# Kernel optimization log

Hardware: AMD Instinct MI355X
Metric: run time of the kernel (lower is better)

Reference implementation:

```python
import jax, jax.numpy as jnp
import numpy as np

HARDLIM_THRESH = 0.2


def setup_inputs() -> dict:
    key = jax.random.key(0)
    k_inp, k_w1, k_b1, k_w2, k_b2 = jax.random.split(key, 5)
    B, D, H, F = 16384, 4096, 2048, 512
    scale1 = 1.0 / np.sqrt(D)
    scale2 = 1.0 / np.sqrt(H)
    return {
        "inp": jax.random.normal(k_inp, (B, D), dtype=jnp.float32),
        "W1": jax.random.normal(k_w1, (H, D), dtype=jnp.float32) * scale1,
        "b1": jax.random.normal(k_b1, (H,), dtype=jnp.float32) * scale1,
        "W2": jax.random.normal(k_w2, (F, H), dtype=jnp.float32) * scale2,
        "b2": jax.random.normal(k_b2, (F,), dtype=jnp.float32) * scale2,
        "k": 8,
    }


def reference(inp, W1, b1, W2, b2, k):
    # Linear -> ReLU -> Linear
    h = jax.nn.relu(inp @ W1.T + b1)            # [B, H]
    logits = h @ W2.T + b2                      # [B, F]
    # 'hard' attention: sigmoid -> keep top-k (zero the rest) -> hardlim(0.2)
    s = jax.nn.sigmoid(logits)
    topk_vals, _ = jax.lax.top_k(s, k)          # [B, k]
    kth = topk_vals[:, -1:]                     # per-row k-th largest value
    gated = jnp.where(s >= kth, s, 0.0)         # GetTopK: zero non-top-k entries
    out = jnp.where(gated > HARDLIM_THRESH, 1.0, 0.0).astype(inp.dtype)
    return out
```

## Files before the change

kernel.cpp:

```cpp
#include <hip/hip_runtime.h>
#include <math.h>
#include <type_traits>


#define BM 128
#define BN 128
#define BK 16

#define TAU   1.0e-4f
#define L02F -1.3862943611198906f

typedef __attribute__((ext_vector_type(8))) short  bf16x8;
typedef __attribute__((ext_vector_type(8))) ushort u16x8;
typedef __attribute__((ext_vector_type(4))) float  f32x4;

__device__ inline ushort bfhi(float f)   { return (ushort)(__float_as_uint(f) >> 16); }
__device__ inline float  bfhif(float f)  { return __uint_as_float(__float_as_uint(f) & 0xFFFF0000u); }

__device__ inline void gload_lds16(const void* g, void* l) {
    __builtin_amdgcn_global_load_lds(
        (const __attribute__((address_space(1))) unsigned int*)g,
        (__attribute__((address_space(3))) unsigned int*)l, 16, 0, 0);
}

__global__ __launch_bounds__(256) void split_kernel(
    const float* __restrict__ src, ushort* __restrict__ hi,
    ushort* __restrict__ lo, size_t n4, int* cnt)
{
    if (cnt && blockIdx.x == 0 && threadIdx.x == 0) *cnt = 0;
    size_t i = (size_t)blockIdx.x * 256 + threadIdx.x;
    size_t stride = (size_t)gridDim.x * 256;
    for (; i < n4; i += stride) {
        float4 v = ((const float4*)src)[i];
        ushort4 h, l;
        h.x = bfhi(v.x); l.x = bfhi(v.x - bfhif(v.x));
        h.y = bfhi(v.y); l.y = bfhi(v.y - bfhif(v.y));
        h.z = bfhi(v.z); l.z = bfhi(v.z - bfhif(v.z));
        h.w = bfhi(v.w); l.w = bfhi(v.w - bfhif(v.w));
        ((ushort4*)hi)[i] = h;
        ((ushort4*)lo)[i] = l;
    }
}

__global__ __launch_bounds__(512, 2) void bgemm1_256(
    const ushort* __restrict__ aH, const ushort* __restrict__ aL,
    const ushort* __restrict__ wH, const ushort* __restrict__ wL,
    const float* __restrict__ b1,
    ushort* __restrict__ Chi, ushort* __restrict__ Clo)
{
    __shared__ ushort lds[65536];
    const int t    = threadIdx.x;
    const int lane = t & 63;
    const int wave = t >> 6;
    const int wr   = wave >> 1;
    const int wc   = wave & 1;
    const int l15  = lane & 15;
    const int l4   = lane >> 4;

    const int bid = blockIdx.x;
    const int xcd = bid & 7;
    const int j   = bid >> 3;
    const int bm  = xcd * 8 + (j >> 3);
    const int bn  = j & 7;

    const int cq = lane & 3;
    const int r0 = wave * 32 + (lane >> 2);
    const int r1 = r0 + 16;
    const size_t sw0 = (size_t)((cq ^ ((r0 >> 1) & 3)) * 8);
    const size_t sw1 = (size_t)((cq ^ ((r1 >> 1) & 3)) * 8);
    const size_t gA0 = (size_t)(bm * 256 + r0) * 4096 + sw0;
    const size_t gA1 = (size_t)(bm * 256 + r1) * 4096 + sw1;
    const size_t gB0 = (size_t)(bn * 256 + r0) * 4096 + sw0;
    const size_t gB1 = (size_t)(bn * 256 + r1) * 4096 + sw1;

    f32x4 acc[4][8];
    #pragma unroll
    for (int mi = 0; mi < 4; ++mi)
        #pragma unroll
        for (int ni = 0; ni < 8; ++ni)
            acc[mi][ni] = (f32x4){0.f, 0.f, 0.f, 0.f};

    auto stage = [&](int b, int kt) {
        const size_t ko = (size_t)kt * 32;
        ushort* L0 = &lds[b * 32768];
        gload_lds16(aH + gA0 + ko, L0 + wave * 1024);
        gload_lds16(aH + gA1 + ko, L0 + wave * 1024 + 512);
        gload_lds16(aL + gA0 + ko, L0 + 8192 + wave * 1024);
        gload_lds16(aL + gA1 + ko, L0 + 8192 + wave * 1024 + 512);
        gload_lds16(wH + gB0 + ko, L0 + 16384 + wave * 1024);
        gload_lds16(wH + gB1 + ko, L0 + 16384 + wave * 1024 + 512);
        gload_lds16(wL + gB0 + ko, L0 + 24576 + wave * 1024);
        gload_lds16(wL + gB1 + ko, L0 + 24576 + wave * 1024 + 512);
    };
    auto compute = [&](int b) {
        const ushort* L0 = &lds[b * 32768];
        bf16x8 ah[4], al[4];
        #pragma unroll
        for (int mi = 0; mi < 4; ++mi) {
            int row = wr * 64 + mi * 16 + l15;
            int o = row * 32 + ((l4 ^ ((row >> 1) & 3)) << 3);
            ah[mi] = *(const bf16x8*)&L0[o];
            al[mi] = *(const bf16x8*)&L0[8192 + o];
        }
        #pragma unroll
        for (int h = 0; h < 2; ++h) {
            bf16x8 bh[4], bl[4];
            #pragma unroll
            for (int q = 0; q < 4; ++q) {
                int row = wc * 128 + (h * 4 + q) * 16 + l15;
                int o = row * 32 + ((l4 ^ ((row >> 1) & 3)) << 3);
                bh[q] = *(const bf16x8*)&L0[16384 + o];
                bl[q] = *(const bf16x8*)&L0[24576 + o];
            }
            __builtin_amdgcn_s_setprio(1);
            #pragma unroll
            for (int mi = 0; mi < 4; ++mi)
                #pragma unroll
                for (int q = 0; q < 4; ++q) {
                    acc[mi][h * 4 + q] = __builtin_amdgcn_mfma_f32_16x16x32_bf16(ah[mi], bh[q], acc[mi][h * 4 + q], 0, 0, 0);
                    acc[mi][h * 4 + q] = __builtin_amdgcn_mfma_f32_16x16x32_bf16(ah[mi], bl[q], acc[mi][h * 4 + q], 0, 0, 0);
                    acc[mi][h * 4 + q] = __builtin_amdgcn_mfma_f32_16x16x32_bf16(al[mi], bh[q], acc[mi][h * 4 + q], 0, 0, 0);
                }
            __builtin_amdgcn_s_setprio(0);
        }
    };

    stage(0, 0);
    asm volatile("s_waitcnt vmcnt(0)");
    __builtin_amdgcn_s_barrier();

    const int nt = 128;
    for (int kt = 0; kt < nt - 1; ++kt) {
        stage((kt + 1) & 1, kt + 1);
        __builtin_amdgcn_sched_barrier(0);
        compute(kt & 1);
        asm volatile("s_waitcnt vmcnt(0)");
        asm volatile("s_waitcnt lgkmcnt(0)\n\ts_barrier" ::: "memory");
    }
    compute((nt - 1) & 1);

    #pragma unroll
    for (int ni = 0; ni < 8; ++ni) {
        int col = bn * 256 + wc * 128 + ni * 16 + l15;
        float bv = b1[col];
        #pragma unroll
        for (int mi = 0; mi < 4; ++mi) {
            int rowb = bm * 256 + wr * 64 + mi * 16 + l4 * 4;
            #pragma unroll
            for (int r = 0; r < 4; ++r) {
                float v = fmaxf(acc[mi][ni][r] + bv, 0.0f);
                size_t idx = (size_t)(rowb + r) * 2048 + col;
                Chi[idx] = bfhi(v);
                Clo[idx] = bfhi(v - bfhif(v));
            }
        }
    }
}

template<int OUT_SPLIT>
__global__ __launch_bounds__(512, 2) void bgemm_glds(
    const ushort* __restrict__ aH, const ushort* __restrict__ aL,
    const ushort* __restrict__ wH, const ushort* __restrict__ wL,
    const float* __restrict__ bias,
    ushort* __restrict__ Chi, ushort* __restrict__ Clo,
    float* __restrict__ C32,
    int N, int K, int nbm, int nbn)
{
    __shared__ ushort lds[73728];
    const int t    = threadIdx.x;
    const int lane = t & 63;
    const int wave = t >> 6;
    const int wr   = wave >> 1;
    const int wc   = wave & 1;
    const int l15  = lane & 15;
    const int l4   = lane >> 4;

    const int bid = blockIdx.x;
    const int xcd = bid & 7;
    const int j   = bid >> 3;
    const int bm  = xcd * (nbm >> 3) + j / nbn;
    const int bn  = j % nbn;

    const int c   = lane & 3;
    const int rA0 = (wave * 2 + 0) * 16 + (lane >> 2);
    const int rA1 = (wave * 2 + 1) * 16 + (lane >> 2);
    const int rB  = wave * 16 + (lane >> 2);
    const size_t offA0 = (size_t)(bm * 256 + rA0) * K + (size_t)((c ^ ((rA0 >> 1) & 3)) * 8);
    const size_t offA1 = (size_t)(bm * 256 + rA1) * K + (size_t)((c ^ ((rA1 >> 1) & 3)) * 8);
    const size_t offB  = (size_t)(bn * 128 + rB ) * K + (size_t)((c ^ ((rB  >> 1) & 3)) * 8);
    const ushort* sAh0 = aH + offA0; const ushort* sAl0 = aL + offA0;
    const ushort* sAh1 = aH + offA1; const ushort* sAl1 = aL + offA1;
    const ushort* sBh  = wH + offB;  const ushort* sBl  = wL + offB;

    f32x4 acc[4][4];
    #pragma unroll
    for (int mi = 0; mi < 4; ++mi)
        #pragma unroll
        for (int ni = 0; ni < 4; ++ni)
            acc[mi][ni] = (f32x4){0.f, 0.f, 0.f, 0.f};

    auto stage = [&](int b, int kt) {
        const size_t ko = (size_t)kt * 32;
        ushort* L0 = &lds[b * 24576];
        gload_lds16(sAh0 + ko, L0 + (wave * 2 + 0) * 512);
        gload_lds16(sAh1 + ko, L0 + (wave * 2 + 1) * 512);
        gload_lds16(sAl0 + ko, L0 + 8192 + (wave * 2 + 0) * 512);
        gload_lds16(sAl1 + ko, L0 + 8192 + (wave * 2 + 1) * 512);
        gload_lds16(sBh + ko,  L0 + 16384 + wave * 512);
        gload_lds16(sBl + ko,  L0 + 20480 + wave * 512);
    };
    auto frag_read = [&](int b, bf16x8 ah[4], bf16x8 al[4], bf16x8 bh[4], bf16x8 bl[4]) {
        const ushort* L0 = &lds[b * 24576];
        #pragma unroll
        for (int mi = 0; mi < 4; ++mi) {
            int row = wr * 64 + mi * 16 + l15;
            int o = row * 32 + ((l4 ^ ((row >> 1) & 3)) << 3);
            ah[mi] = *(const bf16x8*)&L0[o];
            al[mi] = *(const bf16x8*)&L0[8192 + o];
        }
        #pragma unroll
        for (int ni = 0; ni < 4; ++ni) {
            int row = wc * 64 + ni * 16 + l15;
            int o = row * 32 + ((l4 ^ ((row >> 1) & 3)) << 3);
            bh[ni] = *(const bf16x8*)&L0[16384 + o];
            bl[ni] = *(const bf16x8*)&L0[20480 + o];
        }
    };
    auto do_mfma = [&](bf16x8 ah[4], bf16x8 al[4], bf16x8 bh[4], bf16x8 bl[4]) {
        __builtin_amdgcn_s_setprio(1);
        #pragma unroll
        for (int mi = 0; mi < 4; ++mi)
            #pragma unroll
            for (int ni = 0; ni < 4; ++ni) {
                acc[mi][ni] = __builtin_amdgcn_mfma_f32_16x16x32_bf16(ah[mi], bh[ni], acc[mi][ni], 0, 0, 0);
                acc[mi][ni] = __builtin_amdgcn_mfma_f32_16x16x32_bf16(ah[mi], bl[ni], acc[mi][ni], 0, 0, 0);
                acc[mi][ni] = __builtin_amdgcn_mfma_f32_16x16x32_bf16(al[mi], bh[ni], acc[mi][ni], 0, 0, 0);
            }
        __builtin_amdgcn_s_setprio(0);
    };

    stage(0, 0);
    stage(1, 1);
    asm volatile("s_waitcnt vmcnt(6)");
    __builtin_amdgcn_s_barrier();

    const int nt = K / 32;
    bf16x8 ah[4], al[4], bh[4], bl[4];

    for (int kt = 0; kt < nt - 2; ++kt) {
        frag_read(kt % 3, ah, al, bh, bl);
        stage((kt + 2) % 3, kt + 2);
        __builtin_amdgcn_sched_barrier(0);
        do_mfma(ah, al, bh, bl);
        asm volatile("s_waitcnt vmcnt(6)");
        asm volatile("s_waitcnt lgkmcnt(0)\n\ts_barrier" ::: "memory");
    }
    {
        frag_read((nt - 2) % 3, ah, al, bh, bl);
        do_mfma(ah, al, bh, bl);
        asm volatile("s_waitcnt vmcnt(0)");
        asm volatile("s_waitcnt lgkmcnt(0)\n\ts_barrier" ::: "memory");
    }
    {
        frag_read((nt - 1) % 3, ah, al, bh, bl);
        do_mfma(ah, al, bh, bl);
    }

    #pragma unroll
    for (int ni = 0; ni < 4; ++ni) {
        int col = bn * 128 + wc * 64 + ni * 16 + l15;
        float bv = bias[col];
        #pragma unroll
        for (int mi = 0; mi < 4; ++mi) {
            int rowb = bm * 256 + wr * 64 + mi * 16 + l4 * 4;
            #pragma unroll
            for (int r = 0; r < 4; ++r) {
                float v = acc[mi][ni][r] + bv;
                size_t idx = (size_t)(rowb + r) * N + col;
                if (OUT_SPLIT) {
                    v = fmaxf(v, 0.0f);
                    Chi[idx] = bfhi(v);
                    Clo[idx] = bfhi(v - bfhif(v));
                } else {
                    C32[idx] = v;
                }
            }
        }
    }
}

__global__ __launch_bounds__(256) void repair_r1(
    const float* __restrict__ inp,
    const float* __restrict__ W1, const float* __restrict__ b1,
    double* __restrict__ h64,
    const int* __restrict__ risky, const int* __restrict__ cnt, int maxr)
{
    int c = *cnt; if (c > maxr) c = maxr;
    const int by = blockIdx.y;
    if (by * 8 >= c) return;
    __shared__ float Xs[8][4096];
    const int t = threadIdx.x;

    int ridx[8];
    #pragma unroll
    for (int r = 0; r < 8; ++r) {
        int slot = by * 8 + r;
        ridx[r] = risky[slot < c ? slot : (c - 1)];
    }
    #pragma unroll
    for (int i = 0; i < 32; ++i) {
        int lin = t + i * 256;
        int r = lin >> 10, q = lin & 1023;
        *(float4*)&Xs[r][q * 4] = *(const float4*)(inp + (size_t)ridx[r] * 4096 + q * 4);
    }
    __syncthreads();

    const int n0 = blockIdx.x * 256 + t;
    const float* w0 = W1 + (size_t)n0 * 4096;
    double acc[8] = {};

    for (int k = 0; k < 4096; k += 4) {
        float4 a0 = *(const float4*)(w0 + k);
        float xr[8][4];
        #pragma unroll
        for (int r = 0; r < 8; ++r)
            *(float4*)&xr[r][0] = *(const float4*)&Xs[r][k];
        const float* ap0 = &a0.x;
        #pragma unroll
        for (int j = 0; j < 4; ++j) {
            double wd0 = (double)ap0[j];
            #pragma unroll
            for (int r = 0; r < 8; ++r)
                acc[r] = fma(wd0, (double)xr[r][j], acc[r]);
        }
    }

    double bv0 = (double)b1[n0];
    #pragma unroll
    for (int r = 0; r < 8; ++r) {
        int slot = by * 8 + r;
        if (slot < c)
            h64[(size_t)slot * 2048 + n0] = fmax(acc[r] + bv0, 0.0);
    }
}

__global__ __launch_bounds__(256) void repair_r2(
    const double* __restrict__ h64,
    const float* __restrict__ W2, const float* __restrict__ b2,
    double* __restrict__ L64,
    const int* __restrict__ cnt, int maxr)
{
    int c = *cnt; if (c > maxr) c = maxr;
    const int by = blockIdx.y;
    if (by * 4 >= c) return;
    __shared__ double Xs[4][2048];
    const int t = threadIdx.x;

    #pragma unroll
    for (int i = 0; i < 16; ++i) {
        int lin = t + i * 256;
        int r = lin >> 10, q = lin & 1023;
        int slot = by * 4 + r; if (slot >= c) slot = c - 1;
        *(double2*)&Xs[r][q * 2] = *(const double2*)(h64 + (size_t)slot * 2048 + q * 2);
    }
    __syncthreads();

    const int n0 = t;
    const int n1 = t + 256;
    const float* w0 = W2 + (size_t)n0 * 2048;
    const float* w1 = W2 + (size_t)n1 * 2048;
    double acc[2][4] = {};

    for (int k = 0; k < 2048; k += 4) {
        float4 a0 = *(const float4*)(w0 + k);
        float4 a1 = *(const float4*)(w1 + k);
        double xr[4][4];
        #pragma unroll
        for (int r = 0; r < 4; ++r) {
            *(double2*)&xr[r][0] = *(const double2*)&Xs[r][k];
            *(double2*)&xr[r][2] = *(const double2*)&Xs[r][k + 2];
        }
        const float* ap0 = &a0.x;
        const float* ap1 = &a1.x;
        #pragma unroll
        for (int j = 0; j < 4; ++j) {
            double wd0 = (double)ap0[j];
            double wd1 = (double)ap1[j];
            #pragma unroll
            for (int r = 0; r < 4; ++r) {
                acc[0][r] = fma(wd0, xr[r][j], acc[0][r]);
                acc[1][r] = fma(wd1, xr[r][j], acc[1][r]);
            }
        }
    }

    double bv0 = (double)b2[n0], bv1 = (double)b2[n1];
    #pragma unroll
    for (int r = 0; r < 4; ++r) {
        int slot = by * 4 + r;
        if (slot < c) {
            L64[(size_t)slot * 512 + n0] = acc[0][r] + bv0;
            L64[(size_t)slot * 512 + n1] = acc[1][r] + bv1;
        }
    }
}

template<typename TA, int MODE>
__global__ __launch_bounds__(256, 1) void gemm64(
    const TA* __restrict__ A, int lda,
    const float* __restrict__ W, int ldw,
    const float* __restrict__ bias,
    double* __restrict__ out64, int N, int K)
{
    __shared__ double As[BK][BM + 2];
    __shared__ double Bs[BK][BN + 2];
    const int t  = threadIdx.x;
    const int tm = t >> 4;
    const int tn = t & 15;
    const size_t bm = blockIdx.x;
    const size_t bn = blockIdx.y;
    const TA*    Ab = A + bm * BM * (size_t)lda;
    const float* Wb = W + bn * BN * (size_t)ldw;

    double acc[8][8] = {};

    for (int k0 = 0; k0 < K; k0 += BK) {
        #pragma unroll
        for (int i = 0; i < 2; ++i) {
            int f   = t + i * 256;
            int row = f >> 2;
            int kc  = (f & 3) << 2;
            if constexpr (std::is_same<TA, double>::value) {
                double2 v0 = *(const double2*)(Ab + (size_t)row * lda + k0 + kc);
                double2 v1 = *(const double2*)(Ab + (size_t)row * lda + k0 + kc + 2);
                As[kc + 0][row] = v0.x; As[kc + 1][row] = v0.y;
                As[kc + 2][row] = v1.x; As[kc + 3][row] = v1.y;
            } else {
                float4 va = *(const float4*)(Ab + (size_t)row * lda + k0 + kc);
                As[kc + 0][row] = (double)va.x; As[kc + 1][row] = (double)va.y;
                As[kc + 2][row] = (double)va.z; As[kc + 3][row] = (double)va.w;
            }
            float4 vb = *(const float4*)(Wb + (size_t)row * ldw + k0 + kc);
            Bs[kc + 0][row] = (double)vb.x; Bs[kc + 1][row] = (double)vb.y;
            Bs[kc + 2][row] = (double)vb.z; Bs[kc + 3][row] = (double)vb.w;
        }
        __syncthreads();
        #pragma unroll
        for (int k = 0; k < BK; ++k) {
            double a[8], b[8];
            #pragma unroll
            for (int i = 0; i < 4; ++i) {
                *(double2*)&a[i * 2] = *(const double2*)&As[k][tm * 8 + i * 2];
                *(double2*)&b[i * 2] = *(const double2*)&Bs[k][tn * 8 + i * 2];
            }
            #pragma unroll
            for (int i = 0; i < 8; ++i)
                #pragma unroll
                for (int j = 0; j < 8; ++j)
                    acc[i][j] = fma(a[i], b[j], acc[i][j]);
        }
        __syncthreads();
    }

    double bv[8];
    if (MODE != 2) {
        #pragma unroll
        for (int j = 0; j < 8; ++j) bv[j] = (double)bias[bn * BN + tn * 8 + j];
    }

    #pragma unroll
    for (int i = 0; i < 8; ++i) {
        size_t row  = bm * BM + (size_t)tm * 8 + i;
        size_t base = row * (size_t)N + bn * BN + tn * 8;
        #pragma unroll
        for (int j = 0; j < 8; ++j) {
            double v = acc[i][j];
            if (MODE == 0) out64[base + j] = fmax(v + bv[j], 0.0);
            if (MODE == 1) out64[base + j] = v + bv[j];
            if (MODE == 2) out64[base + j] += v;
        }
    }
}

__global__ __launch_bounds__(256) void margin_topk32(
    const float* L, float* O, int ncols,
    const int* __restrict__ kp, int* __restrict__ risky, int* __restrict__ cnt,
    int maxr)
{
    const int wave = threadIdx.x >> 6;
    const int lane = threadIdx.x & 63;
    const int k = *kp;
    const size_t row = (size_t)blockIdx.x * 4 + wave;
    const float* Lr = L + row * (size_t)ncols;

    float v[8];
    *(float4*)&v[0] = *(const float4*)(Lr + lane * 8);
    *(float4*)&v[4] = *(const float4*)(Lr + lane * 8 + 4);
    float w[8];
    #pragma unroll
    for (int j = 0; j < 8; ++j) w[j] = v[j];

    float kth = -3.0e38f, minD = 3.0e38f;
    for (int it = 0; it < k; ++it) {
        float mv = w[0]; int mj = 0;
        #pragma unroll
        for (int j = 1; j < 8; ++j)
            if (w[j] > mv) { mv = w[j]; mj = j; }
        int mi = lane * 8 + mj;
        #pragma unroll
        for (int off = 32; off; off >>= 1) {
            float ov = __shfl_xor(mv, off);
            int   oi = __shfl_xor(mi, off);
            if (ov > mv || (ov == mv && oi < mi)) { mv = ov; mi = oi; }
        }
        kth = mv;
        minD = fminf(minD, fabsf(mv - L02F));
        if ((mi >> 3) == lane) w[mi & 7] = -3.0e38f;
    }
    float nv = w[0];
    #pragma unroll
    for (int j = 1; j < 8; ++j) nv = fmaxf(nv, w[j]);
    #pragma unroll
    for (int off = 32; off; off >>= 1) nv = fmaxf(nv, __shfl_xor(nv, off));

    bool risk = ((kth - nv) < 2.0f * TAU) || (minD < TAU);
    if (risk && lane == 0) {
        int p = atomicAdd(cnt, 1);
        if (p < maxr) risky[p] = (int)row;
    }

    float o[8];
    #pragma unroll
    for (int j = 0; j < 8; ++j)
        o[j] = (v[j] >= kth && v[j] > L02F) ? 1.0f : 0.0f;
    float* Op = O + row * (size_t)ncols + lane * 8;
    *(float4*)&Op[0] = *(const float4*)&o[0];
    *(float4*)&Op[4] = *(const float4*)&o[4];
}

__global__ __launch_bounds__(256) void topk64_kernel(
    const double* __restrict__ L, float* __restrict__ O, int ncols,
    const int* __restrict__ kp,
    const int* __restrict__ risky, const int* __restrict__ cnt, int maxr)
{
    const int wave = threadIdx.x >> 6;
    const int lane = threadIdx.x & 63;
    const int k = *kp;
    size_t pos = (size_t)blockIdx.x * 4 + wave;
    size_t row = pos;
    if (cnt) {
        int c = *cnt; if (c > maxr) c = maxr;
        if ((int)pos >= c) return;
        row = (size_t)risky[pos];
    }
    const double* Lr = L + pos * (size_t)ncols;

    double v[8];
    #pragma unroll
    for (int j = 0; j < 8; ++j) {
        double l = Lr[lane * 8 + j];
        v[j] = 1.0 / (1.0 + exp(-l));
    }
    double w[8];
    #pragma unroll
    for (int j = 0; j < 8; ++j) w[j] = v[j];

    double kth = -1.0e300;
    for (int it = 0; it < k; ++it) {
        double mv = w[0]; int mj = 0;
        #pragma unroll
        for (int j = 1; j < 8; ++j)
            if (w[j] > mv) { mv = w[j]; mj = j; }
        int mi = lane * 8 + mj;
        #pragma unroll
        for (int off = 32; off; off >>= 1) {
            double ov = __shfl_xor(mv, off);
            int    oi = __shfl_xor(mi, off);
            if (ov > mv || (ov == mv && oi < mi)) { mv = ov; mi = oi; }
        }
        kth = mv;
        if ((mi >> 3) == lane) w[mi & 7] = -1.0e300;
    }

    float o[8];
    #pragma unroll
    for (int j = 0; j < 8; ++j)
        o[j] = (v[j] >= kth && v[j] > 0.2) ? 1.0f : 0.0f;
    float* Op = O + row * (size_t)ncols + lane * 8;
    *(float4*)&Op[0] = *(const float4*)&o[0];
    *(float4*)&Op[4] = *(const float4*)&o[4];
}

extern "C" void kernel_launch(void* const* d_in, const int* in_sizes, int n_in,
                              void* d_out, int out_size, void* d_ws, size_t ws_size,
                              hipStream_t stream) {
    const float* inp = (const float*)d_in[0];
    const float* W1  = (const float*)d_in[1];
    const float* b1  = (const float*)d_in[2];
    const float* W2  = (const float*)d_in[3];
    const float* b2  = (const float*)d_in[4];
    const int*   kp  = (const int*)d_in[5];

    const int H = in_sizes[2];
    const int F = in_sizes[4];
    const int D = in_sizes[1] / H;
    const int B = in_sizes[0] / D;
    float* out = (float*)d_out;

    const int MAXR = 8192;
    const size_t szHpair = (size_t)B * H * 4;
    const size_t szW1p   = (size_t)H * D * 4;
    const size_t szW2p   = (size_t)F * H * 4;
    const size_t szInpP  = (size_t)B * D * 4;
    const size_t needMain = szHpair + szW1p + szW2p + (size_t)MAXR * 4 + 256;
    const size_t needA    = needMain + szInpP;
    const bool shapeOK = (D == 4096 && H == 2048 && F == 512 && B == 16384);

    if (shapeOK && ws_size >= needA) {
        ushort* h_hi  = (ushort*)d_ws;
        ushort* h_lo  = h_hi + (size_t)B * H;
        ushort* w1h   = (ushort*)((char*)d_ws + szHpair);
        ushort* w1l   = w1h + (size_t)H * D;
        ushort* w2h   = (ushort*)((char*)d_ws + szHpair + szW1p);
        ushort* w2l   = w2h + (size_t)F * H;
        int*    risky = (int*)((char*)d_ws + szHpair + szW1p + szW2p);
        int*    cnt   = risky + MAXR;
        ushort* inH   = (ushort*)((char*)d_ws + needMain);
        ushort* inL   = inH + (size_t)B * D;
        double* h64   = (double*)d_ws;
        double* L64   = (double*)((char*)d_ws + szHpair);
        float*  l32   = out;

        split_kernel<<<2048, 256, 0, stream>>>(W1, w1h, w1l, (size_t)H * D / 4, cnt);
        split_kernel<<<512, 256, 0, stream>>>(W2, w2h, w2l, (size_t)F * H / 4, nullptr);
        split_kernel<<<4096, 256, 0, stream>>>(inp, inH, inL, (size_t)B * D / 4, nullptr);
        bgemm1_256<<<512, 512, 0, stream>>>(inH, inL, w1h, w1l, b1, h_hi, h_lo);
        bgemm_glds<0><<<256, 512, 0, stream>>>(
            h_hi, h_lo, w2h, w2l, b2, nullptr, nullptr, l32, F, H, B / 256, F / 128);
        margin_topk32<<<B / 4, 256, 0, stream>>>(l32, out, F, kp, risky, cnt, MAXR);
        repair_r1<<<dim3(8, MAXR / 8), 256, 0, stream>>>(
            inp, W1, b1, h64, risky, cnt, MAXR);
        repair_r2<<<dim3(1, MAXR / 4), 256, 0, stream>>>(
            h64, W2, b2, L64, cnt, MAXR);
        topk64_kernel<<<MAXR / 4, 256, 0, stream>>>(L64, out, F, kp, risky, cnt, MAXR);
    } else {
        int Hc = H, Bc = 0;
        for (;;) {
            size_t perRow = (size_t)F * 8 + (size_t)Hc * 8;
            Bc = (int)((ws_size / perRow) / BM) * BM;
            if (Bc >= BM || Hc <= BM) break;
            Hc >>= 1;
        }
        if (Bc < BM) Bc = BM;
        if (Bc > B)  Bc = B;
        double* L   = (double*)d_ws;
        double* h64 = L + (size_t)Bc * F;

        for (int b0 = 0; b0 < B; b0 += Bc) {
            int bc = (B - b0 < Bc) ? (B - b0) : Bc;
            for (int h0 = 0; h0 < H; h0 += Hc) {
                int hc = (H - h0 < Hc) ? (H - h0) : Hc;
                gemm64<float, 0><<<dim3(bc / BM, hc / BN), 256, 0, stream>>>(
                    inp + (size_t)b0 * D, D, W1 + (size_t)h0 * D, D, b1 + h0,
                    h64, hc, D);
                if (h0 == 0)
                    gemm64<double, 1><<<dim3(bc / BM, F / BN), 256, 0, stream>>>(
                        h64, hc, W2 + h0, H, b2, L, F, hc);
                else
                    gemm64<double, 2><<<dim3(bc / BM, F / BN), 256, 0, stream>>>(
                        h64, hc, W2 + h0, H, b2, L, F, hc);
            }
            topk64_kernel<<<bc / 4, 256, 0, stream>>>(
                L, out + (size_t)b0 * F, F, kp, nullptr, nullptr, 0);
        }
    }
}
```

Before: 1.237 ms.

## Load GEMM1 A operand directly into registers, stage only B through LDS

The first GEMM now fetches its A-tile fragments (hi and lo bf16 splits) straight from global memory into VGPRs with inline global_load_dwordx4, instead of staging them through LDS. Only the W1 tile is double-buffered in LDS, which halves shared memory per block and removes the LDS write/read traffic for A. The cost is that each pair of waves sharing a row band loads the same A data redundantly from global/L2. The A loads are also issued in the same iteration they are consumed, with only a partial vmcnt wait, so their latency is exposed rather than prefetched.

```diff
diff --git a/kernel.cpp b/kernel.cpp
--- a/kernel.cpp
+++ b/kernel.cpp
@@ -42,13 +42,13 @@
     }
 }
 
-__global__ __launch_bounds__(512, 2) void bgemm1_256(
+__global__ __launch_bounds__(512, 2) void bgemm1_areg(
     const ushort* __restrict__ aH, const ushort* __restrict__ aL,
     const ushort* __restrict__ wH, const ushort* __restrict__ wL,
     const float* __restrict__ b1,
     ushort* __restrict__ Chi, ushort* __restrict__ Clo)
 {
-    __shared__ ushort lds[65536];
+    __shared__ ushort lds[32768];
     const int t    = threadIdx.x;
     const int lane = t & 63;
     const int wave = t >> 6;
@@ -64,14 +64,13 @@
     const int bn  = j & 7;
 
     const int cq = lane & 3;
-    const int r0 = wave * 32 + (lane >> 2);
-    const int r1 = r0 + 16;
-    const size_t sw0 = (size_t)((cq ^ ((r0 >> 1) & 3)) * 8);
-    const size_t sw1 = (size_t)((cq ^ ((r1 >> 1) & 3)) * 8);
-    const size_t gA0 = (size_t)(bm * 256 + r0) * 4096 + sw0;
-    const size_t gA1 = (size_t)(bm * 256 + r1) * 4096 + sw1;
-    const size_t gB0 = (size_t)(bn * 256 + r0) * 4096 + sw0;
-    const size_t gB1 = (size_t)(bn * 256 + r1) * 4096 + sw1;
+    const int rs0 = wave * 32 + (lane >> 2);
+    const int rs1 = rs0 + 16;
+    const size_t gB0 = (size_t)(bn * 256 + rs0) * 4096 + (size_t)((cq ^ ((rs0 >> 1) & 3)) * 8);
+    const size_t gB1 = (size_t)(bn * 256 + rs1) * 4096 + (size_t)((cq ^ ((rs1 >> 1) & 3)) * 8);
+
+    const ushort* aHb = aH + ((size_t)(bm * 256 + wr * 64 + l15)) * 4096 + l4 * 8;
+    const ushort* aLb = aL + ((size_t)(bm * 256 + wr * 64 + l15)) * 4096 + l4 * 8;
 
     f32x4 acc[4][8];
     #pragma unroll
@@ -80,64 +79,76 @@
         for (int ni = 0; ni < 8; ++ni)
             acc[mi][ni] = (f32x4){0.f, 0.f, 0.f, 0.f};
 
-    auto stage = [&](int b, int kt) {
+    auto stageB = [&](int b, int kt) {
         const size_t ko = (size_t)kt * 32;
-        ushort* L0 = &lds[b * 32768];
-        gload_lds16(aH + gA0 + ko, L0 + wave * 1024);
-        gload_lds16(aH + gA1 + ko, L0 + wave * 1024 + 512);
-        gload_lds16(aL + gA0 + ko, L0 + 8192 + wave * 1024);
-        gload_lds16(aL + gA1 + ko, L0 + 8192 + wave * 1024 + 512);
-        gload_lds16(wH + gB0 + ko, L0 + 16384 + wave * 1024);
-        gload_lds16(wH + gB1 + ko, L0 + 16384 + wave * 1024 + 512);
-        gload_lds16(wL + gB0 + ko, L0 + 24576 + wave * 1024);
-        gload_lds16(wL + gB1 + ko, L0 + 24576 + wave * 1024 + 512);
+        ushort* L0 = &lds[b * 16384];
+        gload_lds16(wH + gB0 + ko, L0 + wave * 1024);
+        gload_lds16(wH + gB1 + ko, L0 + wave * 1024 + 512);
+        gload_lds16(wL + gB0 + ko, L0 + 8192 + wave * 1024);
+        gload_lds16(wL + gB1 + ko, L0 + 8192 + wave * 1024 + 512);
     };
-    auto compute = [&](int b) {
-        const ushort* L0 = &lds[b * 32768];
-        bf16x8 ah[4], al[4];
+    auto a_load = [&](int kt, bf16x8 av[8]) {
+        const size_t ko = (size_t)kt * 32;
         #pragma unroll
         for (int mi = 0; mi < 4; ++mi) {
-            int row = wr * 64 + mi * 16 + l15;
+            asm volatile("global_load_dwordx4 %0, %1, off"
+                         : "=v"(av[mi])     : "v"(aHb + ko + (size_t)mi * 65536));
+            asm volatile("global_load_dwordx4 %0, %1, off"
+                         : "=v"(av[4 + mi]) : "v"(aLb + ko + (size_t)mi * 65536));
+        }
+    };
+    auto mfma_half = [&](int b, int h, bf16x8 av[8]) {
+        const ushort* L0 = &lds[b * 16384];
+        bf16x8 bh[4], bl[4];
+        #pragma unroll
+        for (int q = 0; q < 4; ++q) {
+            int row = wc * 128 + (h * 4 + q) * 16 + l15;
             int o = row * 32 + ((l4 ^ ((row >> 1) & 3)) << 3);
-            ah[mi] = *(const bf16x8*)&L0[o];
-            al[mi] = *(const bf16x8*)&L0[8192 + o];
-        }
-        #pragma unroll
-        for (int h = 0; h < 2; ++h) {
-            bf16x8 bh[4], bl[4];
+            bh[q] = *(const bf16x8*)&L0[o];
+            bl[q] = *(const bf16x8*)&L0[8192 + o];
+        }
+        __builtin_amdgcn_s_setprio(1);
+        #pragma unroll
+        for (int mi = 0; mi < 4; ++mi)
             #pragma unroll
             for (int q = 0; q < 4; ++q) {
-                int row = wc * 128 + (h * 4 + q) * 16 + l15;
-                int o = row * 32 + ((l4 ^ ((row >> 1) & 3)) << 3);
-                bh[q] = *(const bf16x8*)&L0[16384 + o];
-                bl[q] = *(const bf16x8*)&L0[24576 + o];
-            }
-            __builtin_amdgcn_s_setprio(1);
-            #pragma unroll
-            for (int mi = 0; mi < 4; ++mi)
-                #pragma unroll
-                for (int q = 0; q < 4; ++q) {
-                    acc[mi][h * 4 + q] = __builtin_amdgcn_mfma_f32_16x16x32_bf16(ah[mi], bh[q], acc[mi][h * 4 + q], 0, 0, 0);
-                    acc[mi][h * 4 + q] = __builtin_amdgcn_mfma_f32_16x16x32_bf16(ah[mi], bl[q], acc[mi][h * 4 + q], 0, 0, 0);
-                    acc[mi][h * 4 + q] = __builtin_amdgcn_mfma_f32_16x16x32_bf16(al[mi], bh[q], acc[mi][h * 4 + q], 0, 0, 0);
-                }
-            __builtin_amdgcn_s_setprio(0);
-        }
+                acc[mi][h * 4 + q] = __builtin_amdgcn_mfma_f32_16x16x32_bf16(av[mi],     bh[q], acc[mi][h * 4 + q], 0, 0, 0);
+                acc[mi][h * 4 + q] = __builtin_amdgcn_mfma_f32_16x16x32_bf16(av[mi],     bl[q], acc[mi][h * 4 + q], 0, 0, 0);
+                acc[mi][h * 4 + q] = __builtin_amdgcn_mfma_f32_16x16x32_bf16(av[4 + mi], bh[q], acc[mi][h * 4 + q], 0, 0, 0);
+            }
+        __builtin_amdgcn_s_setprio(0);
     };
-
-    stage(0, 0);
+    #define KEEP8(a) asm volatile("" : "+v"(a[0]), "+v"(a[1]), "+v"(a[2]), "+v"(a[3]), \
+                                       "+v"(a[4]), "+v"(a[5]), "+v"(a[6]), "+v"(a[7]))
+
+    stageB(0, 0);
     asm volatile("s_waitcnt vmcnt(0)");
     __builtin_amdgcn_s_barrier();
 
     const int nt = 128;
+    bf16x8 av[8];
+
     for (int kt = 0; kt < nt - 1; ++kt) {
-        stage((kt + 1) & 1, kt + 1);
+        a_load(kt, av);
         __builtin_amdgcn_sched_barrier(0);
-        compute(kt & 1);
+        stageB((kt + 1) & 1, kt + 1);
+        __builtin_amdgcn_sched_barrier(0);
+        asm volatile("s_waitcnt vmcnt(4)");
+        KEEP8(av);
+        __builtin_amdgcn_sched_barrier(0);
+        mfma_half(kt & 1, 0, av);
+        mfma_half(kt & 1, 1, av);
         asm volatile("s_waitcnt vmcnt(0)");
         asm volatile("s_waitcnt lgkmcnt(0)\n\ts_barrier" ::: "memory");
     }
-    compute((nt - 1) & 1);
+    {
+        a_load(nt - 1, av);
+        asm volatile("s_waitcnt vmcnt(0)");
+        KEEP8(av);
+        __builtin_amdgcn_sched_barrier(0);
+        mfma_half((nt - 1) & 1, 0, av);
+        mfma_half((nt - 1) & 1, 1, av);
+    }
 
     #pragma unroll
     for (int ni = 0; ni < 8; ++ni) {
@@ -155,6 +166,7 @@
             }
         }
     }
+    #undef KEEP8
 }
 
 template<int OUT_SPLIT>
@@ -634,7 +646,7 @@
         split_kernel<<<2048, 256, 0, stream>>>(W1, w1h, w1l, (size_t)H * D / 4, cnt);
         split_kernel<<<512, 256, 0, stream>>>(W2, w2h, w2l, (size_t)F * H / 4, nullptr);
         split_kernel<<<4096, 256, 0, stream>>>(inp, inH, inL, (size_t)B * D / 4, nullptr);
-        bgemm1_256<<<512, 512, 0, stream>>>(inH, inL, w1h, w1l, b1, h_hi, h_lo);
+        bgemm1_areg<<<512, 512, 0, stream>>>(inH, inL, w1h, w1l, b1, h_hi, h_lo);
         bgemm_glds<0><<<256, 512, 0, stream>>>(
             h_hi, h_lo, w2h, w2l, b2, nullptr, nullptr, l32, F, H, B / 256, F / 128);
         margin_topk32<<<B / 4, 256, 0, stream>>>(l32, out, F, kp, risky, cnt, MAXR);
```

After: 1.498 ms. +21.1%, slower.
